# Performance work log

Measured on AMD Instinct MI355X. Metric: run time of the kernel, lower is better.

The kernel has to match this reference:

```python
import jax, jax.numpy as jnp
import numpy as np

# ---- config (matches init_kwargs) ----
B, S, V = 8, 900, 11
H, NH, HD = 512, 8, 64          # hidden, heads, head_dim = H // NH
L = 2                            # num_layers
EXPANSION = 4.0
INNER = 1536                     # find_multiple(round(4.0 * 512 * 2/3), 256)
STEPS = 2                        # mcmc_num_steps
EPS = 1e-5                       # rms_norm_eps
THETA = 10000.0                  # rope_theta
ESCALE = float(np.sqrt(H))       # embed_scale = sqrt(hidden_size)
SCALE = 1.0 / float(np.sqrt(HD))


def rms_norm(x):
    return x * jax.lax.rsqrt(jnp.mean(x * x, axis=-1, keepdims=True) + EPS)


def rope_tables():
    inv_freq = 1.0 / (THETA ** (jnp.arange(0, HD, 2, dtype=jnp.float32) / HD))
    t = jnp.arange(S, dtype=jnp.float32)
    freqs = jnp.outer(t, inv_freq)                # (S, HD/2)
    emb = jnp.concatenate([freqs, freqs], axis=-1)  # (S, HD)
    return jnp.cos(emb), jnp.sin(emb)


def rotate_half(x):
    x1, x2 = jnp.split(x, 2, axis=-1)
    return jnp.concatenate([-x2, x1], axis=-1)


def apply_rope(q, k, cos, sin):
    cos = cos[None, :, None, :]  # (1,S,1,HD) broadcast over batch & heads
    sin = sin[None, :, None, :]
    return q * cos + rotate_half(q) * sin, k * cos + rotate_half(k) * sin


def block(h, qkv_w, o_w, gu_w, d_w, cos, sin):
    b, s, _ = h.shape
    qkv = (h @ qkv_w).reshape(b, s, 3 * NH, HD)
    q, k, v = qkv[:, :, :NH], qkv[:, :, NH:2 * NH], qkv[:, :, 2 * NH:]
    q, k = apply_rope(q, k, cos, sin)
    scores = jnp.einsum('bqhd,bkhd->bhqk', q, k) * SCALE
    attn = jax.nn.softmax(scores, axis=-1)
    out = jnp.einsum('bhqk,bkhd->bqhd', attn, v).reshape(b, s, NH * HD)
    h = rms_norm(h + out @ o_w)                   # post-norm residual
    gu = h @ gu_w
    gate, up = gu[..., :INNER], gu[..., INNER:]
    h = rms_norm(h + (jax.nn.silu(gate) * up) @ d_w)
    return h


def energy(logits, embed_w, energy_w, qkv_w, o_w, gu_w, d_w, input_emb, cos, sin):
    probs = jax.nn.softmax(logits, axis=-1)       # soft token distribution
    h = input_emb + ESCALE * (probs @ embed_w)    # soft embedding
    for i in range(L):
        h = block(h, qkv_w[i], o_w[i], gu_w[i], d_w[i], cos, sin)
    return jnp.sum(h @ energy_w)                  # scalar energy


def setup_inputs() -> dict:
    key = jax.random.key(0)
    ks = jax.random.split(key, 8)
    inputs = jax.random.randint(ks[0], (B, S), 0, V, dtype=jnp.int64)
    puzzle_identifiers = jax.random.randint(ks[1], (B,), 0, 1, dtype=jnp.int64)
    init_std = 1.0 / ESCALE
    embed_w = jax.random.normal(ks[2], (V, H), jnp.float32) * init_std
    energy_w = jax.random.normal(ks[3], (H, 1), jnp.float32) * 0.02
    qkv_w = jax.random.normal(ks[4], (L, H, 3 * NH * HD), jnp.float32) * 0.02
    o_w = jax.random.normal(ks[5], (L, NH * HD, H), jnp.float32) * 0.02
    gu_w = jax.random.normal(ks[6], (L, H, 2 * INNER), jnp.float32) * 0.02
    d_w = jax.random.normal(ks[7], (L, INNER, H), jnp.float32) * 0.02
    alpha = jnp.asarray(100.0, jnp.float32)       # mcmc_step_size
    return {"inputs": inputs, "puzzle_identifiers": puzzle_identifiers,
            "embed_w": embed_w, "energy_w": energy_w, "qkv_w": qkv_w,
            "o_w": o_w, "gu_w": gu_w, "d_w": d_w, "alpha": alpha}


def reference(inputs, puzzle_identifiers, embed_w, energy_w, qkv_w, o_w, gu_w, d_w, alpha):
    cos, sin = rope_tables()
    input_emb = ESCALE * embed_w[inputs]          # (B,S,H)
    a = jnp.maximum(alpha, 1e-4)                  # torch.clamp(alpha, min=1e-4)
    logits = jnp.zeros((inputs.shape[0], S, V), jnp.float32)
    egrad = jax.grad(energy)
    for _ in range(STEPS):                        # MCMC energy-descent loop
        g = egrad(logits, embed_w, energy_w, qkv_w, o_w, gu_w, d_w, input_emb, cos, sin)
        logits = logits - a * g
    return logits
```

## Files before the change

### kernel.cpp

```cpp
#include <hip/hip_runtime.h>
#include <math.h>

#define B_ 8
#define S_ 900
#define V_ 11
#define H_ 512
#define NH_ 8
#define HD_ 64
#define INNER_ 1536
#define STEPS_ 2
#define NTOK (B_*S_)
#define EPS_ 1e-5f
#define THETA_ 10000.0f
#define ESCALE_ 22.627416997969522f
#define SCALE_ 0.125f
#define PT_ 68

typedef __attribute__((ext_vector_type(8))) short bh8;
typedef __attribute__((ext_vector_type(4))) float f32x4;
typedef __attribute__((ext_vector_type(4))) unsigned short us4;

union bfu { bh8 v; unsigned short s[8]; us4 q[2]; };

__device__ inline unsigned short f2bf(float x) {
// ... 74 lines not shown
  if (tid < V_) p[tid] = P[t * V_ + tid];
  if (tid == 0) iw = inp[t];
  __syncthreads();
  for (int h = tid; h < H_; h += blockDim.x) {
    float acc = E[iw * H_ + h];
#pragma unroll
    for (int v = 0; v < V_; ++v) acc += p[v] * E[v * H_ + h];
    float val = ESCALE_ * acc;
    h0[(size_t)t * H_ + h] = val;
    h016[(size_t)t * H_ + h] = f2bf(val);
  }
}

__global__ void k_gfill(const float* __restrict__ ew, float* __restrict__ G) {
  int idx = blockIdx.x * blockDim.x + threadIdx.x;
  if (idx < NTOK * H_) G[idx] = ew[idx & (H_ - 1)];
}

__global__ void k_cast8(const float* __restrict__ X, unsigned short* __restrict__ Y, int n8) {
  int i = blockIdx.x * blockDim.x + threadIdx.x;
  if (i >= n8) return;
  const float4* p = (const float4*)(X + (size_t)i * 8);
  float4 a = p[0], b = p[1];
  bfu o;
  o.s[0] = f2bf(a.x); o.s[1] = f2bf(a.y); o.s[2] = f2bf(a.z); o.s[3] = f2bf(a.w);
  o.s[4] = f2bf(b.x); o.s[5] = f2bf(b.y); o.s[6] = f2bf(b.z); o.s[7] = f2bf(b.w);
  *(bh8*)(Y + (size_t)i * 8) = o.v;
}


__global__ void k_wt(const float* __restrict__ W, unsigned short* __restrict__ WT, int K, int N) {
  __shared__ float t[32][33];
  int k0 = blockIdx.y * 32, n0 = blockIdx.x * 32;
  int tx = threadIdx.x, ty = threadIdx.y;
#pragma unroll
  for (int i = 0; i < 4; ++i)
    t[ty + 8 * i][tx] = W[(size_t)(k0 + ty + 8 * i) * N + n0 + tx];
  __syncthreads();
#pragma unroll
  for (int i = 0; i < 4; ++i)
    WT[(size_t)(n0 + ty + 8 * i) * K + k0 + tx] = f2bf(t[tx][ty + 8 * i]);
}


template <int TM, int SILU_A, int ADD, int CBF, int ROPE, int SILUBWD>
__global__ __launch_bounds__(256) void k_gemm(const unsigned short* __restrict__ A16,
                                              const unsigned short* __restrict__ Bt,
                                              const float* __restrict__ Dm,
                                              float* __restrict__ Cf,
                                              unsigned short* __restrict__ C16,
                                              unsigned short* __restrict__ GU,
                                              const float* __restrict__ Cs,
                                              const float* __restrict__ Sn,
                                              int M, int N, int K, int lda) {
  __shared__ unsigned short As[2][TM][32];
  __shared__ unsigned short Bs[2][128][32];
  constexpr int FR = TM / 32;
  int tid = threadIdx.x;
  int m0 = blockIdx.y * TM, n0 = blockIdx.x * 128;
  int wid = tid >> 6, lane = tid & 63;
  int wr = (wid >> 1) * (FR * 16), wc = (wid & 1) * 64;
  int lr = lane & 15, lg = lane >> 4;
  int srow = lane >> 2, sck = (lane & 3) * 8;
  f32x4 acc[FR][4] = {};
  for (int k0 = 0; k0 < K; k0 += 64) {
    __syncthreads();
#pragma unroll
    for (int sub = 0; sub < 2; ++sub) {
      int kk = k0 + sub * 32;
#pragma unroll
      for (int half = 0; half < TM / 64; ++half) {
        if (SILU_A) {
          int row = (tid >> 2) + 64 * half;
          int ck = (tid & 3) * 8;
          int gr = m0 + row; gr = gr < M ? gr : M - 1;
          const unsigned short* src = &A16[(size_t)gr * lda + kk + ck];
          bfu pa;
#pragma unroll
          for (int j = 0; j < 8; ++j) {
            float g = b2f(src[j]), u = b2f(src[INNER_ + j]);
            pa.s[j] = f2bf((g / (1.f + __expf(-g))) * u);
          }
          *(bh8*)&As[sub][row][ck] = pa.v;
        } else {
          int gr = m0 + 64 * half + wid * 16 + srow; gr = gr < M ? gr : M - 1;
          gld16(&A16[(size_t)gr * lda + kk + sck], &As[sub][64 * half + wid * 16][0]);
        }
      }
#pragma unroll
      for (int i = 0; i < 2; ++i) {
        int bb = wid * 2 + i;
        gld16(&Bt[(size_t)(n0 + bb * 16 + srow) * K + kk + sck], &Bs[sub][bb * 16][0]);
      }
    }
    __syncthreads();
#pragma unroll
    for (int sub = 0; sub < 2; ++sub) {
      bh8 av[FR], bv[4];
#pragma unroll
      for (int fr = 0; fr < FR; ++fr) av[fr] = *(const bh8*)&As[sub][wr + fr * 16 + lr][lg * 8];
#pragma unroll
      for (int fc = 0; fc < 4; ++fc) bv[fc] = *(const bh8*)&Bs[sub][wc + fc * 16 + lr][lg * 8];
#pragma unroll
      for (int fr = 0; fr < FR; ++fr)
#pragma unroll
        for (int fc = 0; fc < 4; ++fc)
          acc[fr][fc] = __builtin_amdgcn_mfma_f32_16x16x32_bf16(av[fr], bv[fc], acc[fr][fc], 0, 0, 0);
    }
  }
  bool rope_on = ROPE && (((n0 + wc) >> 6) < 16);
#pragma unroll
  for (int fr = 0; fr < FR; ++fr) {
    int r0 = m0 + wr + fr * 16 + lg * 4;
#pragma unroll
    for (int i = 0; i < 4; ++i) {
      int gr = r0 + i;
      if (gr >= M) continue;
      float c0 = 1.f, s0 = 0.f, c1 = 1.f, s1 = 0.f;
      if (ROPE) {
        if (rope_on) {
          int s = gr % S_;
          c0 = Cs[s * 32 + lr];      s0 = Sn[s * 32 + lr];
          c1 = Cs[s * 32 + 16 + lr]; s1 = Sn[s * 32 + 16 + lr];
        }
      }
#pragma unroll
      for (int fc = 0; fc < 4; ++fc) {
        int gc = n0 + wc + fc * 16 + lr;
        float out = acc[fr][fc][i];
        if (ROPE) {
          float part = acc[fr][fc ^ 2][i];
          float cc = (fc & 1) ? c1 : c0;
          float ss = (fc & 1) ? s1 : s0;
          out = (fc < 2) ? (out * cc - part * ss) : (out * cc + part * ss);
        }
        if (ADD) out += Dm[(size_t)gr * N + gc];
        if (SILUBWD) {
          size_t gb = (size_t)gr * (size_t)(2 * INNER_) + gc;
          float g = b2f(GU[gb]), u = b2f(GU[gb + INNER_]);
          float sig = 1.f / (1.f + __expf(-g));
          GU[gb] = f2bf(out * u * sig * (1.f + g * (1.f - sig)));
          GU[gb + INNER_] = f2bf(out * g * sig);
        } else if (CBF) {
          C16[(size_t)gr * N + gc] = f2bf(out);
        } else {
          Cf[(size_t)gr * N + gc] = out;
        }
      }
    }
  }
}


__global__ __launch_bounds__(256) void k_attn_fwd3(const unsigned short* __restrict__ QKV,
                                                   unsigned short* __restrict__ AO,
                                                   float* __restrict__ MB,
                                                   float* __restrict__ LB) {
  __shared__ unsigned short Ks[64][PT_];
  __shared__ unsigned short VT[64][PT_];
  __shared__ unsigned short Ps[4][16][PT_];
  int tid = threadIdx.x;
  int h = blockIdx.y, b = blockIdx.z;
  int w = tid >> 6, lane = tid & 63;
  int lr = lane & 15, lg = lane >> 4;
  int q0 = blockIdx.x * 64 + w * 16;
  int sr = tid >> 2, sc0 = (tid & 3) * 16;
  int vd0 = (tid & 15) * 4, vk0 = (tid >> 4) * 4;

  bh8 qf[2];
  {
    int qr = q0 + lr; if (qr >= S_) qr = S_ - 1;
    const unsigned short* qp = &QKV[((size_t)(b * S_ + qr) * 24 + h) * 64 + lg * 8];
    qf[0] = *(const bh8*)qp;
    qf[1] = *(const bh8*)(qp + 32);
  }
  f32x4 accO[4] = {};
  float m[4], lsum[4];
#pragma unroll
  for (int i = 0; i < 4; ++i) { m[i] = -1e30f; lsum[i] = 0.f; }

  bfu kA, kB;
  us4 vR[4];
  {
    int src = sr;
    size_t ts = (size_t)b * S_ + (src < S_ ? src : S_ - 1);
    const unsigned short* gp = &QKV[(ts * 24 + 8 + h) * 64 + sc0];
    kA.v = *(const bh8*)gp;
    kB.v = *(const bh8*)(gp + 8);
#pragma unroll
    for (int j = 0; j < 4; ++j) {
      int s2 = vk0 + j;
      size_t t2 = (size_t)b * S_ + (s2 < S_ ? s2 : S_ - 1);
      vR[j] = *(const us4*)&QKV[(t2 * 24 + 16 + h) * 64 + vd0];
    }
  }

  for (int kt = 0; kt < S_; kt += 64) {
    __syncthreads();
    sts16(&Ks[sr][sc0], kA);
    sts16(&Ks[sr][sc0 + 8], kB);
#pragma unroll
    for (int dd = 0; dd < 4; ++dd) {
      us4 pk = {vR[0][dd], vR[1][dd], vR[2][dd], vR[3][dd]};
      *(us4*)&VT[vd0 + dd][vk0] = pk;
    }
    __syncthreads();
    if (kt + 64 < S_) {
      int src = kt + 64 + sr;
      size_t ts = (size_t)b * S_ + (src < S_ ? src : S_ - 1);
      const unsigned short* gp = &QKV[(ts * 24 + 8 + h) * 64 + sc0];
      kA.v = *(const bh8*)gp;
      kB.v = *(const bh8*)(gp + 8);
#pragma unroll
      for (int j = 0; j < 4; ++j) {
        int s2 = kt + 64 + vk0 + j;
        size_t t2 = (size_t)b * S_ + (s2 < S_ ? s2 : S_ - 1);
        vR[j] = *(const us4*)&QKV[(t2 * 24 + 16 + h) * 64 + vd0];
      }
    }
    f32x4 accS[4] = {};
#pragma unroll
    for (int ks = 0; ks < 2; ++ks)
#pragma unroll
      for (int fk = 0; fk < 4; ++fk)
        accS[fk] = __builtin_amdgcn_mfma_f32_16x16x32_bf16(qf[ks], lds16(&Ks[fk * 16 + lr][ks * 32 + lg * 8]), accS[fk], 0, 0, 0);
    float sc[4][4], pmax[4];
#pragma unroll
    for (int i = 0; i < 4; ++i) pmax[i] = -1e30f;
#pragma unroll
    for (int fk = 0; fk < 4; ++fk)
#pragma unroll
      for (int i = 0; i < 4; ++i) {
        float s = accS[fk][i] * SCALE_;
        if (kt + fk * 16 + lr >= S_) s = -1e30f;
        sc[fk][i] = s;
        pmax[i] = fmaxf(pmax[i], s);
      }
#pragma unroll
    for (int i = 0; i < 4; ++i) {
      float v = pmax[i];
      v = fmaxf(v, __shfl_xor(v, 1, 64));
      v = fmaxf(v, __shfl_xor(v, 2, 64));
      v = fmaxf(v, __shfl_xor(v, 4, 64));
      v = fmaxf(v, __shfl_xor(v, 8, 64));
      pmax[i] = v;
    }
    float psum[4];
#pragma unroll
    for (int i = 0; i < 4; ++i) {
      float mn = fmaxf(m[i], pmax[i]);
      float eo = __expf(m[i] - mn);
      m[i] = mn;
      lsum[i] *= eo;
#pragma unroll
      for (int fd = 0; fd < 4; ++fd) accO[fd][i] *= eo;
      psum[i] = 0.f;
    }
#pragma unroll
    for (int fk = 0; fk < 4; ++fk)
#pragma unroll
      for (int i = 0; i < 4; ++i) {
        float p = __expf(sc[fk][i] - m[i]);
        sc[fk][i] = p;
        psum[i] += p;
      }
#pragma unroll
    for (int i = 0; i < 4; ++i) {
      float v = psum[i];
      v += __shfl_xor(v, 1, 64);
      v += __shfl_xor(v, 2, 64);
      v += __shfl_xor(v, 4, 64);
      v += __shfl_xor(v, 8, 64);
      lsum[i] += v;
    }
#pragma unroll
    for (int fk = 0; fk < 4; ++fk)
#pragma unroll
      for (int i = 0; i < 4; ++i)
        Ps[w][lg * 4 + i][fk * 16 + lr] = f2bf(sc[fk][i]);
#pragma unroll
    for (int ks = 0; ks < 2; ++ks) {
      bh8 ap = lds16(&Ps[w][lr][ks * 32 + lg * 8]);
#pragma unroll
      for (int fd = 0; fd < 4; ++fd)
        accO[fd] = __builtin_amdgcn_mfma_f32_16x16x32_bf16(ap, lds16(&VT[fd * 16 + lr][ks * 32 + lg * 8]), accO[fd], 0, 0, 0);
    }
  }
#pragma unroll
  for (int i = 0; i < 4; ++i) {
    int q = q0 + lg * 4 + i;
    if (q < S_) {
      float linv = 1.f / lsum[i];
      size_t obase = (size_t)(b * S_ + q) * H_ + h * 64;
#pragma unroll
      for (int fd = 0; fd < 4; ++fd) AO[obase + fd * 16 + lr] = f2bf(accO[fd][i] * linv);
      if (lr == 0) {
        MB[((size_t)b * NH_ + h) * S_ + q] = m[i];
        LB[((size_t)b * NH_ + h) * S_ + q] = linv;
      }
    }
  }
}

__global__ __launch_bounds__(256) void k_delta(const unsigned short* __restrict__ O,
                                               const unsigned short* __restrict__ dO,
                                               float* __restrict__ DB) {
  int tid = threadIdx.x;
  int h = blockIdx.y, b = blockIdx.z;
  int r = blockIdx.x * 64 + (tid >> 2), part = tid & 3;
  if (r >= S_) return;
  size_t base = (size_t)(b * S_ + r) * H_ + h * 64 + part * 16;
  bfu o0, o1, d0, d1;
  o0.v = *(const bh8*)&O[base];  o1.v = *(const bh8*)&O[base + 8];
  d0.v = *(const bh8*)&dO[base]; d1.v = *(const bh8*)&dO[base + 8];
  float s = 0.f;
#pragma unroll
  for (int j = 0; j < 8; ++j)
    s += b2f(o0.s[j]) * b2f(d0.s[j]) + b2f(o1.s[j]) * b2f(d1.s[j]);
  s = quad_sum(s);
  if (part == 0) DB[((size_t)b * NH_ + h) * S_ + r] = s;
}

__global__ __launch_bounds__(256) void k_attn_bwd_dq3(const unsigned short* __restrict__ QKV,
                                                      const unsigned short* __restrict__ dO,
                                                      const float* __restrict__ MB,
                                                      const float* __restrict__ LB,
                                                      const float* __restrict__ DB,
                                                      const float* __restrict__ Cs,
                                                      const float* __restrict__ Sn,
                                                      unsigned short* __restrict__ dQKV) {
  __shared__ unsigned short Ks[64][PT_];
  __shared__ unsigned short Vs[64][PT_];
  __shared__ unsigned short KT[64][PT_];
  __shared__ unsigned short Ps[4][16][PT_];
  int tid = threadIdx.x;
  int h = blockIdx.y, b = blockIdx.z;
  int w = tid >> 6, lane = tid & 63;
  int lr = lane & 15, lg = lane >> 4;
  int q0 = blockIdx.x * 64 + w * 16;
  size_t sbase = ((size_t)b * NH_ + h) * S_;
  int sr = tid >> 2, sc0 = (tid & 3) * 16;
  int vd0 = (tid & 15) * 4, vk0 = (tid >> 4) * 4;

  bh8 qf[2], dof[2];
  {
    int qr = q0 + lr; if (qr >= S_) qr = S_ - 1;
    const unsigned short* qp = &QKV[((size_t)(b * S_ + qr) * 24 + h) * 64 + lg * 8];
    const unsigned short* dp = &dO[(size_t)(b * S_ + qr) * H_ + h * 64 + lg * 8];
    qf[0] = *(const bh8*)qp;  qf[1] = *(const bh8*)(qp + 32);
    dof[0] = *(const bh8*)dp; dof[1] = *(const bh8*)(dp + 32);
  }
  float mrow[4], lrow[4], drow[4];
#pragma unroll
  for (int i = 0; i < 4; ++i) {
    int q = q0 + lg * 4 + i; if (q >= S_) q = S_ - 1;
    mrow[i] = MB[sbase + q];
    lrow[i] = LB[sbase + q];
    drow[i] = DB[sbase + q];
  }
  f32x4 accQ[4] = {};

  bfu pA{}, pB{}, pC{}, pD{};
  us4 rv[4];
  {
    int src = sr;
    bool vld = src < S_;
    size_t ts = (size_t)b * S_ + (vld ? src : S_ - 1);
    const unsigned short* kp = &QKV[(ts * 24 + 8 + h) * 64 + sc0];
    if (vld) {
      pA.v = *(const bh8*)kp;
      pB.v = *(const bh8*)(kp + 8);
      pC.v = *(const bh8*)(kp + 512);
      pD.v = *(const bh8*)(kp + 520);
    }
#pragma unroll
    for (int j = 0; j < 4; ++j) {
      int s2 = vk0 + j;
      bool v2 = s2 < S_;
      size_t t2 = (size_t)b * S_ + (v2 ? s2 : S_ - 1);
      us4 t = *(const us4*)&QKV[(t2 * 24 + 8 + h) * 64 + vd0];
      if (!v2) t = us4{0, 0, 0, 0};
      rv[j] = t;
    }
  }

  for (int kt = 0; kt < S_; kt += 64) {
    __syncthreads();
    sts16(&Ks[sr][sc0], pA); sts16(&Ks[sr][sc0 + 8], pB);
    sts16(&Vs[sr][sc0], pC); sts16(&Vs[sr][sc0 + 8], pD);
#pragma unroll
    for (int dd = 0; dd < 4; ++dd) {
      us4 pk = {rv[0][dd], rv[1][dd], rv[2][dd], rv[3][dd]};
      *(us4*)&KT[vd0 + dd][vk0] = pk;
    }
    __syncthreads();
    if (kt + 64 < S_) {
      int src = kt + 64 + sr;
      bool vld = src < S_;
      size_t ts = (size_t)b * S_ + (vld ? src : S_ - 1);
      const unsigned short* kp = &QKV[(ts * 24 + 8 + h) * 64 + sc0];
      pA = bfu{}; pB = bfu{}; pC = bfu{}; pD = bfu{};
      if (vld) {
        pA.v = *(const bh8*)kp;
        pB.v = *(const bh8*)(kp + 8);
        pC.v = *(const bh8*)(kp + 512);
        pD.v = *(const bh8*)(kp + 520);
      }
#pragma unroll
      for (int j = 0; j < 4; ++j) {
        int s2 = kt + 64 + vk0 + j;
        bool v2 = s2 < S_;
        size_t t2 = (size_t)b * S_ + (v2 ? s2 : S_ - 1);
        us4 t = *(const us4*)&QKV[(t2 * 24 + 8 + h) * 64 + vd0];
        if (!v2) t = us4{0, 0, 0, 0};
        rv[j] = t;
      }
    }
    f32x4 aS[4] = {}, aD[4] = {};
#pragma unroll
    for (int ks = 0; ks < 2; ++ks)
#pragma unroll
      for (int fk = 0; fk < 4; ++fk) {
        aS[fk] = __builtin_amdgcn_mfma_f32_16x16x32_bf16(qf[ks], lds16(&Ks[fk * 16 + lr][ks * 32 + lg * 8]), aS[fk], 0, 0, 0);
        aD[fk] = __builtin_amdgcn_mfma_f32_16x16x32_bf16(dof[ks], lds16(&Vs[fk * 16 + lr][ks * 32 + lg * 8]), aD[fk], 0, 0, 0);
      }
#pragma unroll
    for (int fk = 0; fk < 4; ++fk)
#pragma unroll
      for (int i = 0; i < 4; ++i) {
        float p = __expf(aS[fk][i] * SCALE_ - mrow[i]) * lrow[i];
        float ds = p * (aD[fk][i] - drow[i]);
        Ps[w][lg * 4 + i][fk * 16 + lr] = f2bf(ds);
      }
#pragma unroll
    for (int ks = 0; ks < 2; ++ks) {
      bh8 ap = lds16(&Ps[w][lr][ks * 32 + lg * 8]);
#pragma unroll
      for (int fd = 0; fd < 4; ++fd)
        accQ[fd] = __builtin_amdgcn_mfma_f32_16x16x32_bf16(ap, lds16(&KT[fd * 16 + lr][ks * 32 + lg * 8]), accQ[fd], 0, 0, 0);
    }
  }
#pragma unroll
  for (int i = 0; i < 4; ++i) {
    int q = q0 + lg * 4 + i;
    if (q < S_) {
      size_t obase = ((size_t)(b * S_ + q) * 24 + h) * 64;
      float c0 = Cs[q * 32 + lr], s0 = Sn[q * 32 + lr];
      float c1 = Cs[q * 32 + 16 + lr], s1 = Sn[q * 32 + 16 + lr];
#pragma unroll
      for (int fd = 0; fd < 4; ++fd) {
        float x = SCALE_ * accQ[fd][i];
        float p = SCALE_ * accQ[fd ^ 2][i];
        float cc = (fd & 1) ? c1 : c0;
        float ss = (fd & 1) ? s1 : s0;
        float out = (fd < 2) ? (x * cc + p * ss) : (x * cc - p * ss);
        dQKV[obase + fd * 16 + lr] = f2bf(out);
      }
    }
  }
}

__global__ __launch_bounds__(256) void k_attn_bwd_kv3(const unsigned short* __restrict__ QKV,
                                                      const unsigned short* __restrict__ dO,
                                                      const float* __restrict__ MB,
                                                      const float* __restrict__ LB,
                                                      const float* __restrict__ DB,
                                                      const float* __restrict__ Cs,
                                                      const float* __restrict__ Sn,
                                                      unsigned short* __restrict__ dQKV) {
  __shared__ unsigned short Qs[64][PT_];
  __shared__ unsigned short dOs[64][PT_];
  __shared__ unsigned short QT[64][PT_];
  __shared__ unsigned short dOT[64][PT_];
  __shared__ unsigned short Ps[4][16][PT_];
  __shared__ float sM[64], sL[64], sD[64];
  int tid = threadIdx.x;
  int h = blockIdx.y, b = blockIdx.z;
  int w = tid >> 6, lane = tid & 63;
  int lr = lane & 15, lg = lane >> 4;
  int k0w = blockIdx.x * 64 + w * 16;
  size_t sbase = ((size_t)b * NH_ + h) * S_;
  int sr = tid >> 2, sc0 = (tid & 3) * 16;
  int vd0 = (tid & 15) * 4, vk0 = (tid >> 4) * 4;

  bh8 kf[2], vf[2];
  {
    int kr = k0w + lr; if (kr >= S_) kr = S_ - 1;
    const unsigned short* kp = &QKV[((size_t)(b * S_ + kr) * 24 + 8 + h) * 64 + lg * 8];
    kf[0] = *(const bh8*)kp;        kf[1] = *(const bh8*)(kp + 32);
    vf[0] = *(const bh8*)(kp + 512); vf[1] = *(const bh8*)(kp + 544);
  }
  f32x4 accK[4] = {}, accV[4] = {};

  bfu pA, pB, pC{}, pD{};
  us4 rq[4], rd[4];
  float stM = 0.f, stL = 0.f, stD = 0.f;
  {
    int src = sr;
    bool vld = src < S_;
    size_t ts = (size_t)b * S_ + (vld ? src : S_ - 1);
    const unsigned short* qp = &QKV[(ts * 24 + h) * 64 + sc0];
    const unsigned short* dp = &dO[ts * H_ + h * 64 + sc0];
    pA.v = *(const bh8*)qp;
    pB.v = *(const bh8*)(qp + 8);
    if (vld) {
      pC.v = *(const bh8*)dp;
      pD.v = *(const bh8*)(dp + 8);
    }
#pragma unroll
    for (int j = 0; j < 4; ++j) {
      int s2 = vk0 + j;
      bool v2 = s2 < S_;
      size_t t2 = (size_t)b * S_ + (v2 ? s2 : S_ - 1);
      rq[j] = *(const us4*)&QKV[(t2 * 24 + h) * 64 + vd0];
      us4 td = *(const us4*)&dO[t2 * H_ + h * 64 + vd0];
      if (!v2) td = us4{0, 0, 0, 0};
      rd[j] = td;
    }
    if (tid < 64) {
      bool v2 = tid < S_;
      int sc = v2 ? tid : S_ - 1;
      stM = MB[sbase + sc];
      stL = LB[sbase + sc];
      stD = v2 ? DB[sbase + sc] : 0.f;
    }
  }

  for (int qt = 0; qt < S_; qt += 64) {
    __syncthreads();
    sts16(&Qs[sr][sc0], pA);  sts16(&Qs[sr][sc0 + 8], pB);
    sts16(&dOs[sr][sc0], pC); sts16(&dOs[sr][sc0 + 8], pD);
#pragma unroll
    for (int dd = 0; dd < 4; ++dd) {
      us4 pq = {rq[0][dd], rq[1][dd], rq[2][dd], rq[3][dd]};
      us4 pd = {rd[0][dd], rd[1][dd], rd[2][dd], rd[3][dd]};
      *(us4*)&QT[vd0 + dd][vk0] = pq;
      *(us4*)&dOT[vd0 + dd][vk0] = pd;
    }
    if (tid < 64) {
      sM[tid] = stM;
      sL[tid] = stL;
      sD[tid] = stD;
    }
    __syncthreads();
    if (qt + 64 < S_) {
      int src = qt + 64 + sr;
      bool vld = src < S_;
      size_t ts = (size_t)b * S_ + (vld ? src : S_ - 1);
      const unsigned short* qp = &QKV[(ts * 24 + h) * 64 + sc0];
      const unsigned short* dp = &dO[ts * H_ + h * 64 + sc0];
      pA.v = *(const bh8*)qp;
      pB.v = *(const bh8*)(qp + 8);
      pC = bfu{}; pD = bfu{};
      if (vld) {
        pC.v = *(const bh8*)dp;
        pD.v = *(const bh8*)(dp + 8);
      }
#pragma unroll
      for (int j = 0; j < 4; ++j) {
        int s2 = qt + 64 + vk0 + j;
        bool v2 = s2 < S_;
        size_t t2 = (size_t)b * S_ + (v2 ? s2 : S_ - 1);
        rq[j] = *(const us4*)&QKV[(t2 * 24 + h) * 64 + vd0];
        us4 td = *(const us4*)&dO[t2 * H_ + h * 64 + vd0];
        if (!v2) td = us4{0, 0, 0, 0};
        rd[j] = td;
      }
      if (tid < 64) {
        int s2 = qt + 64 + tid;
        bool v2 = s2 < S_;
        int sc = v2 ? s2 : S_ - 1;
        stM = MB[sbase + sc];
        stL = LB[sbase + sc];
        stD = v2 ? DB[sbase + sc] : 0.f;
      }
    }
    f32x4 aS[4] = {}, aD[4] = {};
#pragma unroll
    for (int ks = 0; ks < 2; ++ks)
#pragma unroll
      for (int fq = 0; fq < 4; ++fq) {
        aS[fq] = __builtin_amdgcn_mfma_f32_16x16x32_bf16(kf[ks], lds16(&Qs[fq * 16 + lr][ks * 32 + lg * 8]), aS[fq], 0, 0, 0);
        aD[fq] = __builtin_amdgcn_mfma_f32_16x16x32_bf16(vf[ks], lds16(&dOs[fq * 16 + lr][ks * 32 + lg * 8]), aD[fq], 0, 0, 0);
      }
    float pv[4][4];
#pragma unroll
    for (int fq = 0; fq < 4; ++fq) {
      float mq = sM[fq * 16 + lr], lq = sL[fq * 16 + lr];
#pragma unroll
      for (int i = 0; i < 4; ++i) {
        float p = __expf(aS[fq][i] * SCALE_ - mq) * lq;
        pv[fq][i] = p;
        Ps[w][lg * 4 + i][fq * 16 + lr] = f2bf(p);
      }
    }
#pragma unroll
    for (int qs = 0; qs < 2; ++qs) {
      bh8 ap = lds16(&Ps[w][lr][qs * 32 + lg * 8]);
#pragma unroll
      for (int fd = 0; fd < 4; ++fd)
        accV[fd] = __builtin_amdgcn_mfma_f32_16x16x32_bf16(ap, lds16(&dOT[fd * 16 + lr][qs * 32 + lg * 8]), accV[fd], 0, 0, 0);
    }
#pragma unroll
    for (int fq = 0; fq < 4; ++fq) {
      float dq = sD[fq * 16 + lr];
#pragma unroll
      for (int i = 0; i < 4; ++i)
        Ps[w][lg * 4 + i][fq * 16 + lr] = f2bf(pv[fq][i] * (aD[fq][i] - dq));
    }
#pragma unroll
    for (int qs = 0; qs < 2; ++qs) {
      bh8 ap = lds16(&Ps[w][lr][qs * 32 + lg * 8]);
#pragma unroll
      for (int fd = 0; fd < 4; ++fd)
        accK[fd] = __builtin_amdgcn_mfma_f32_16x16x32_bf16(ap, lds16(&QT[fd * 16 + lr][qs * 32 + lg * 8]), accK[fd], 0, 0, 0);
    }
  }
#pragma unroll
  for (int i = 0; i < 4; ++i) {
    int k = k0w + lg * 4 + i;
    if (k < S_) {
      size_t obase = ((size_t)(b * S_ + k) * 24 + 8 + h) * 64;
      float c0 = Cs[k * 32 + lr], s0 = Sn[k * 32 + lr];
      float c1 = Cs[k * 32 + 16 + lr], s1 = Sn[k * 32 + 16 + lr];
#pragma unroll
      for (int fd = 0; fd < 4; ++fd) {
        float x = SCALE_ * accK[fd][i];
        float p = SCALE_ * accK[fd ^ 2][i];
        float cc = (fd & 1) ? c1 : c0;
        float ss = (fd & 1) ? s1 : s0;
        float out = (fd < 2) ? (x * cc + p * ss) : (x * cc - p * ss);
        dQKV[obase + fd * 16 + lr] = f2bf(out);
        dQKV[obase + 512 + fd * 16 + lr] = f2bf(accV[fd][i]);
      }
    }
  }
}


__global__ __launch_bounds__(256) void k_rms_fwd(const float* __restrict__ X, float* __restrict__ Y,
                                                 unsigned short* __restrict__ Y16) {
  int t = blockIdx.x, tid = threadIdx.x;
  float x0 = X[(size_t)t * H_ + tid], x1 = X[(size_t)t * H_ + tid + 256];
  __shared__ float red[256];
  red[tid] = x0 * x0 + x1 * x1;
  __syncthreads();
  for (int s = 128; s > 0; s >>= 1) {
    if (tid < s) red[tid] += red[tid + s];
    __syncthreads();
  }
  float r = rsqrtf(red[0] / H_ + EPS_);
  float y0 = x0 * r, y1 = x1 * r;
  Y[(size_t)t * H_ + tid] = y0;
  Y[(size_t)t * H_ + tid + 256] = y1;
  Y16[(size_t)t * H_ + tid] = f2bf(y0);
  Y16[(size_t)t * H_ + tid + 256] = f2bf(y1);
}

__global__ __launch_bounds__(256) void k_rms_bwd(const float* __restrict__ X,
                                                 const float* __restrict__ GY,
                                                 float* __restrict__ GX,
                                                 unsigned short* __restrict__ GX16) {
  int t = blockIdx.x, tid = threadIdx.x;
  float x0 = X[(size_t)t * H_ + tid], x1 = X[(size_t)t * H_ + tid + 256];
  float g0 = GY[(size_t)t * H_ + tid], g1 = GY[(size_t)t * H_ + tid + 256];
  __shared__ float r1[256], r2[256];
  r1[tid] = x0 * x0 + x1 * x1;
  r2[tid] = x0 * g0 + x1 * g1;
  __syncthreads();
  for (int s = 128; s > 0; s >>= 1) {
    if (tid < s) { r1[tid] += r1[tid + s]; r2[tid] += r2[tid + s]; }
    __syncthreads();
  }
  float r = rsqrtf(r1[0] / H_ + EPS_);
  float coef = r * r * r * r2[0] / (float)H_;
  float o0 = r * g0 - coef * x0, o1 = r * g1 - coef * x1;
  GX[(size_t)t * H_ + tid] = o0;
  GX[(size_t)t * H_ + tid + 256] = o1;
  GX16[(size_t)t * H_ + tid] = f2bf(o0);
  GX16[(size_t)t * H_ + tid + 256] = f2bf(o1);
}


__global__ __launch_bounds__(64) void k_logits_update(const float* __restrict__ G,
                                                      const float* __restrict__ E,
                                                      const float* __restrict__ P,
                                                      const float* __restrict__ alpha,
                                                      float* __restrict__ logits) {
  int t = blockIdx.x, lane = threadIdx.x;
  float dp[V_];
#pragma unroll
  for (int v = 0; v < V_; ++v) dp[v] = 0.f;
  for (int hh = lane; hh < H_; hh += 64) {
    float gh = G[(size_t)t * H_ + hh];
#pragma unroll
    for (int v = 0; v < V_; ++v) dp[v] += gh * E[v * H_ + hh];
  }
#pragma unroll
  for (int v = 0; v < V_; ++v) dp[v] = wave_sum64(dp[v]) * ESCALE_;
  float dot = 0.f;
  float pv[V_];
#pragma unroll
  for (int v = 0; v < V_; ++v) {
    pv[v] = P[t * V_ + v];
    dot += pv[v] * dp[v];
  }
  float a = fmaxf(alpha[0], 1e-4f);
  if (lane < V_) logits[t * V_ + lane] -= a * pv[lane] * (dp[lane] - dot);
}


struct Ctx {
  unsigned short *Q16, *Q016, *dQ16, *GU16, *DO16, *AO16, *AO016, *X116, *UDX16, *U016;
  float *X1, *X2, *X20, *G, *UDX, *P, *MB, *LB, *DB, *MB0, *LB0, *CS, *SN;
  const unsigned short *WTqkv[2], *WTo[2], *WTgu[2], *WTd[2];
  const unsigned short *WSqkv[2], *WSo[2], *WSgu[2], *WSd[2];
  hipStream_t st;
};

static void block_forward(Ctx& c, int l, const float* hin, const unsigned short* hin16,
                          float* hout, unsigned short* qb, unsigned short* ao,
                          float* mb, float* lb, float* x2buf, unsigned short* u16buf) {
  k_gemm<128, 0, 0, 1, 1, 0><<<dim3(3 * H_ / 128, (NTOK + 127) / 128), 256, 0, c.st>>>(
      hin16, c.WTqkv[l], nullptr, nullptr, qb, nullptr, c.CS, c.SN, NTOK, 3 * H_, H_, H_);
  k_attn_fwd3<<<dim3((S_ + 63) / 64, NH_, B_), 256, 0, c.st>>>(qb, ao, mb, lb);
  k_gemm<64, 0, 1, 0, 0, 0><<<dim3(H_ / 128, (NTOK + 63) / 64), 256, 0, c.st>>>(
      ao, c.WTo[l], hin, c.X1, nullptr, nullptr, nullptr, nullptr, NTOK, H_, H_, H_);
  k_rms_fwd<<<NTOK, 256, 0, c.st>>>(c.X1, c.UDX, u16buf);
  k_gemm<128, 0, 0, 1, 0, 0><<<dim3(2 * INNER_ / 128, (NTOK + 127) / 128), 256, 0, c.st>>>(
      u16buf, c.WTgu[l], nullptr, nullptr, c.GU16, nullptr, nullptr, nullptr, NTOK, 2 * INNER_, H_, H_);
  k_gemm<64, 1, 1, 0, 0, 0><<<dim3(H_ / 128, (NTOK + 63) / 64), 256, 0, c.st>>>(
      c.GU16, c.WTd[l], c.UDX, x2buf, nullptr, nullptr, nullptr, nullptr, NTOK, H_, INNER_, 2 * INNER_);
  if (hout) k_rms_fwd<<<NTOK, 256, 0, c.st>>>(x2buf, hout, c.UDX16);
}

static void block_backward(Ctx& c, int l, const float* hin, const unsigned short* hin16,
                           unsigned short* qb, unsigned short* ao, float* mb, float* lb,
                           bool full) {
  const float* x2src;
  if (full) {
    block_forward(c, l, hin, hin16, nullptr, qb, ao, mb, lb, c.X2, c.UDX16);
    x2src = c.X2;
  } else {
    k_gemm<64, 0, 1, 0, 0, 0><<<dim3(H_ / 128, (NTOK + 63) / 64), 256, 0, c.st>>>(
        ao, c.WTo[l], hin, c.X1, nullptr, nullptr, nullptr, nullptr, NTOK, H_, H_, H_);
    k_gemm<128, 0, 0, 1, 0, 0><<<dim3(2 * INNER_ / 128, (NTOK + 127) / 128), 256, 0, c.st>>>(
        c.U016, c.WTgu[l], nullptr, nullptr, c.GU16, nullptr, nullptr, nullptr, NTOK, 2 * INNER_, H_, H_);
    x2src = c.X20;
  }
  k_rms_bwd<<<NTOK, 256, 0, c.st>>>(x2src, c.G, c.UDX, c.UDX16);
  k_gemm<128, 0, 0, 0, 0, 1><<<dim3(INNER_ / 128, (NTOK + 127) / 128), 256, 0, c.st>>>(
      c.UDX16, c.WSd[l], nullptr, nullptr, nullptr, c.GU16, nullptr, nullptr, NTOK, INNER_, H_, H_);
  k_gemm<64, 0, 1, 0, 0, 0><<<dim3(H_ / 128, (NTOK + 63) / 64), 256, 0, c.st>>>(
      c.GU16, c.WSgu[l], c.UDX, c.G, nullptr, nullptr, nullptr, nullptr, NTOK, H_, 2 * INNER_, 2 * INNER_);
  k_rms_bwd<<<NTOK, 256, 0, c.st>>>(c.X1, c.G, c.UDX, c.UDX16);
  k_gemm<64, 0, 0, 1, 0, 0><<<dim3(H_ / 128, (NTOK + 63) / 64), 256, 0, c.st>>>(
      c.UDX16, c.WSo[l], nullptr, nullptr, c.DO16, nullptr, nullptr, nullptr, NTOK, H_, H_, H_);
  dim3 agrid((S_ + 63) / 64, NH_, B_);
  k_delta<<<agrid, 256, 0, c.st>>>(ao, c.DO16, c.DB);
  k_attn_bwd_dq3<<<agrid, 256, 0, c.st>>>(qb, c.DO16, mb, lb, c.DB, c.CS, c.SN, c.dQ16);
  k_attn_bwd_kv3<<<agrid, 256, 0, c.st>>>(qb, c.DO16, mb, lb, c.DB, c.CS, c.SN, c.dQ16);
  k_gemm<64, 0, 1, 0, 0, 0><<<dim3(H_ / 128, (NTOK + 63) / 64), 256, 0, c.st>>>(
      c.dQ16, c.WSqkv[l], c.UDX, c.G, nullptr, nullptr, nullptr, nullptr, NTOK, H_, 3 * H_, 3 * H_);
}

extern "C" void kernel_launch(void* const* d_in, const int* in_sizes, int n_in,
                              void* d_out, int out_size, void* d_ws, size_t ws_size,
                              hipStream_t stream) {
  const int* inputs = (const int*)d_in[0];
  const float* E = (const float*)d_in[2];
  const float* ew = (const float*)d_in[3];
  const float* qkvw = (const float*)d_in[4];
  const float* ow = (const float*)d_in[5];
  const float* guw = (const float*)d_in[6];
  const float* dw = (const float*)d_in[7];
  const float* alpha = (const float*)d_in[8];
  float* logits = (float*)d_out;

  const size_t WT_FLOATS = 3407872;
  const size_t NEED =
      3 * ((size_t)NTOK * 3 * H_ / 2) +
      ((size_t)NTOK * INNER_) +
      5 * ((size_t)NTOK * H_) +
      6 * ((size_t)NTOK * H_ / 2) +
      ((size_t)NTOK * V_) +
      5 * ((size_t)B_ * NH_ * S_) +
      2 * ((size_t)S_ * 32) +
      2 * WT_FLOATS;
  if (ws_size < NEED * sizeof(float)) {
    k_zero<<<(NTOK * V_ + 255) / 256, 256, 0, stream>>>(logits, NTOK * V_);
    return;
  }

  float* f = (float*)d_ws;
  Ctx c;
  c.st = stream;
  c.Q16 = (unsigned short*)f;  f += (size_t)NTOK * 3 * H_ / 2;
  c.Q016 = (unsigned short*)f; f += (size_t)NTOK * 3 * H_ / 2;
  c.dQ16 = (unsigned short*)f; f += (size_t)NTOK * 3 * H_ / 2;
  c.GU16 = (unsigned short*)f; f += (size_t)NTOK * INNER_;
  c.X1 = f;   f += (size_t)NTOK * H_;
  c.X2 = f;   f += (size_t)NTOK * H_;
  c.X20 = f;  f += (size_t)NTOK * H_;
  c.G = f;    f += (size_t)NTOK * H_;
  c.UDX = f;  f += (size_t)NTOK * H_;
  c.AO16 = (unsigned short*)f;  f += (size_t)NTOK * H_ / 2;
  c.AO016 = (unsigned short*)f; f += (size_t)NTOK * H_ / 2;
  c.DO16 = (unsigned short*)f;  f += (size_t)NTOK * H_ / 2;
  c.X116 = (unsigned short*)f;  f += (size_t)NTOK * H_ / 2;
  c.UDX16 = (unsigned short*)f; f += (size_t)NTOK * H_ / 2;
  c.U016 = (unsigned short*)f;  f += (size_t)NTOK * H_ / 2;
  c.P = f;    f += (size_t)NTOK * V_;
  c.MB = f;   f += (size_t)B_ * NH_ * S_;
  c.LB = f;   f += (size_t)B_ * NH_ * S_;
  c.DB = f;   f += (size_t)B_ * NH_ * S_;
  c.MB0 = f;  f += (size_t)B_ * NH_ * S_;
  c.LB0 = f;  f += (size_t)B_ * NH_ * S_;
  c.CS = f;   f += (size_t)S_ * 32;
  c.SN = f;   f += (size_t)S_ * 32;
  unsigned short* wt = (unsigned short*)f;

  const size_t LQKV = (size_t)H_ * 3 * H_;
  const size_t LO = (size_t)H_ * H_;
  const size_t LGU = (size_t)H_ * 2 * INNER_;
  const size_t LD = (size_t)INNER_ * H_;

  for (int l = 0; l < 2; ++l) {
    c.WTqkv[l] = wt;
    k_wt<<<dim3(3 * H_ / 32, H_ / 32), dim3(32, 8), 0, stream>>>(qkvw + l * LQKV, wt, H_, 3 * H_);
    wt += LQKV;
    c.WTo[l] = wt;
    k_wt<<<dim3(H_ / 32, H_ / 32), dim3(32, 8), 0, stream>>>(ow + l * LO, wt, H_, H_);
    wt += LO;
    c.WTgu[l] = wt;
    k_wt<<<dim3(2 * INNER_ / 32, H_ / 32), dim3(32, 8), 0, stream>>>(guw + l * LGU, wt, H_, 2 * INNER_);
    wt += LGU;
    c.WTd[l] = wt;
    k_wt<<<dim3(H_ / 32, INNER_ / 32), dim3(32, 8), 0, stream>>>(dw + l * LD, wt, INNER_, H_);
    wt += LD;
  }
  {
    unsigned short* ws = wt;
    k_cast8<<<(int)((2 * LQKV / 8 + 255) / 256), 256, 0, stream>>>(qkvw, ws, (int)(2 * LQKV / 8));
    c.WSqkv[0] = ws; c.WSqkv[1] = ws + LQKV; ws += 2 * LQKV;
    k_cast8<<<(int)((2 * LO / 8 + 255) / 256), 256, 0, stream>>>(ow, ws, (int)(2 * LO / 8));
    c.WSo[0] = ws; c.WSo[1] = ws + LO; ws += 2 * LO;
    k_cast8<<<(int)((2 * LGU / 8 + 255) / 256), 256, 0, stream>>>(guw, ws, (int)(2 * LGU / 8));
    c.WSgu[0] = ws; c.WSgu[1] = ws + LGU; ws += 2 * LGU;
    k_cast8<<<(int)((2 * LD / 8 + 255) / 256), 256, 0, stream>>>(dw, ws, (int)(2 * LD / 8));
    c.WSd[0] = ws; c.WSd[1] = ws + LD;
  }

  k_zero<<<(NTOK * V_ + 255) / 256, 256, 0, stream>>>(logits, NTOK * V_);
  k_rope_tables<<<(S_ * 32 + 255) / 256, 256, 0, stream>>>(c.CS, c.SN);

  for (int step = 0; step < STEPS_; ++step) {
    k_softmax_logits<<<(NTOK + 255) / 256, 256, 0, stream>>>(logits, c.P);
    k_h0<<<NTOK, 256, 0, stream>>>(c.P, E, inputs, c.X1, c.X116);
    block_forward(c, 0, c.X1, c.X116, c.UDX, c.Q016, c.AO016, c.MB0, c.LB0, c.X20, c.U016);
    k_gfill<<<(NTOK * H_ + 255) / 256, 256, 0, stream>>>(ew, c.G);
    block_backward(c, 1, c.UDX, c.UDX16, c.Q16, c.AO16, c.MB, c.LB, true);
    k_h0<<<NTOK, 256, 0, stream>>>(c.P, E, inputs, c.X1, c.X116);
    block_backward(c, 0, c.X1, c.X116, c.Q016, c.AO016, c.MB0, c.LB0, false);
    k_logits_update<<<NTOK, 64, 0, stream>>>(c.G, E, c.P, alpha, logits);
  }
}
```

Measured before the change: 2.356 ms.

## Double attention query tile to 128 rows with 512-thread blocks and split K/V staging roles

The forward, dQ and dKV attention kernels now run 8 waves per block over 128 query (or key) rows instead of 4 waves over 64. Each K/V tile staged in shared memory is therefore reused by twice as many waves. The staging work is split so the first 256 threads load the row-major tile and the other 256 build the transposed tile, which halves the per-thread load work. In exchange there are fewer blocks (8 per head instead of 15), a larger tail on the last tile, and more register and shared-memory pressure at 512 threads per block.

```diff
diff --git a/kernel.cpp b/kernel.cpp
--- a/kernel.cpp
+++ b/kernel.cpp
@@ -250,20 +250,22 @@
 }
 
 
-__global__ __launch_bounds__(256) void k_attn_fwd3(const unsigned short* __restrict__ QKV,
+__global__ __launch_bounds__(512) void k_attn_fwd3(const unsigned short* __restrict__ QKV,
                                                    unsigned short* __restrict__ AO,
                                                    float* __restrict__ MB,
                                                    float* __restrict__ LB) {
   __shared__ unsigned short Ks[64][PT_];
   __shared__ unsigned short VT[64][PT_];
-  __shared__ unsigned short Ps[4][16][PT_];
+  __shared__ unsigned short Ps[8][16][PT_];
   int tid = threadIdx.x;
   int h = blockIdx.y, b = blockIdx.z;
   int w = tid >> 6, lane = tid & 63;
   int lr = lane & 15, lg = lane >> 4;
-  int q0 = blockIdx.x * 64 + w * 16;
-  int sr = tid >> 2, sc0 = (tid & 3) * 16;
-  int vd0 = (tid & 15) * 4, vk0 = (tid >> 4) * 4;
+  int q0 = blockIdx.x * 128 + w * 16;
+  bool kRole = tid < 256;
+  int t2 = kRole ? tid : tid - 256;
+  int sr = t2 >> 2, sc0 = (t2 & 3) * 16;
+  int vd0 = (t2 & 15) * 4, vk0 = (t2 >> 4) * 4;
 
   bh8 qf[2];
   {
@@ -279,41 +281,48 @@
 
   bfu kA, kB;
   us4 vR[4];
-  {
+  if (kRole) {
     int src = sr;
     size_t ts = (size_t)b * S_ + (src < S_ ? src : S_ - 1);
     const unsigned short* gp = &QKV[(ts * 24 + 8 + h) * 64 + sc0];
     kA.v = *(const bh8*)gp;
     kB.v = *(const bh8*)(gp + 8);
+  } else {
 #pragma unroll
     for (int j = 0; j < 4; ++j) {
       int s2 = vk0 + j;
-      size_t t2 = (size_t)b * S_ + (s2 < S_ ? s2 : S_ - 1);
-      vR[j] = *(const us4*)&QKV[(t2 * 24 + 16 + h) * 64 + vd0];
+      size_t t3 = (size_t)b * S_ + (s2 < S_ ? s2 : S_ - 1);
+      vR[j] = *(const us4*)&QKV[(t3 * 24 + 16 + h) * 64 + vd0];
     }
   }
 
   for (int kt = 0; kt < S_; kt += 64) {
     __syncthreads();
-    sts16(&Ks[sr][sc0], kA);
-    sts16(&Ks[sr][sc0 + 8], kB);
-#pragma unroll
-    for (int dd = 0; dd < 4; ++dd) {
-      us4 pk = {vR[0][dd], vR[1][dd], vR[2][dd], vR[3][dd]};
-      *(us4*)&VT[vd0 + dd][vk0] = pk;
+    if (kRole) {
+      sts16(&Ks[sr][sc0], kA);
+      sts16(&Ks[sr][sc0 + 8], kB);
+    } else {
+#pragma unroll
+      for (int dd = 0; dd < 4; ++dd) {
+        us4 pk = {vR[0][dd], vR[1][dd], vR[2][dd], vR[3][dd]};
+        *(us4*)&VT[vd0 + dd][vk0] = pk;
+      }
     }
     __syncthreads();
     if (kt + 64 < S_) {
-      int src = kt + 64 + sr;
-      size_t ts = (size_t)b * S_ + (src < S_ ? src : S_ - 1);
-      const unsigned short* gp = &QKV[(ts * 24 + 8 + h) * 64 + sc0];
-      kA.v = *(const bh8*)gp;
-      kB.v = *(const bh8*)(gp + 8);
-#pragma unroll
-      for (int j = 0; j < 4; ++j) {
-        int s2 = kt + 64 + vk0 + j;
-        size_t t2 = (size_t)b * S_ + (s2 < S_ ? s2 : S_ - 1);
-        vR[j] = *(const us4*)&QKV[(t2 * 24 + 16 + h) * 64 + vd0];
+      if (kRole) {
+        int src = kt + 64 + sr;
+        size_t ts = (size_t)b * S_ + (src < S_ ? src : S_ - 1);
+        const unsigned short* gp = &QKV[(ts * 24 + 8 + h) * 64 + sc0];
+        kA.v = *(const bh8*)gp;
+        kB.v = *(const bh8*)(gp + 8);
+      } else {
+#pragma unroll
+        for (int j = 0; j < 4; ++j) {
+          int s2 = kt + 64 + vk0 + j;
+          size_t t3 = (size_t)b * S_ + (s2 < S_ ? s2 : S_ - 1);
+          vR[j] = *(const us4*)&QKV[(t3 * 24 + 16 + h) * 64 + vd0];
+        }
       }
     }
     f32x4 accS[4] = {};
@@ -419,7 +428,7 @@
   if (part == 0) DB[((size_t)b * NH_ + h) * S_ + r] = s;
 }
 
-__global__ __launch_bounds__(256) void k_attn_bwd_dq3(const unsigned short* __restrict__ QKV,
+__global__ __launch_bounds__(512) void k_attn_bwd_dq3(const unsigned short* __restrict__ QKV,
                                                       const unsigned short* __restrict__ dO,
                                                       const float* __restrict__ MB,
                                                       const float* __restrict__ LB,
@@ -430,15 +439,17 @@
   __shared__ unsigned short Ks[64][PT_];
   __shared__ unsigned short Vs[64][PT_];
   __shared__ unsigned short KT[64][PT_];
-  __shared__ unsigned short Ps[4][16][PT_];
+  __shared__ unsigned short Ps[8][16][PT_];
   int tid = threadIdx.x;
   int h = blockIdx.y, b = blockIdx.z;
   int w = tid >> 6, lane = tid & 63;
   int lr = lane & 15, lg = lane >> 4;
-  int q0 = blockIdx.x * 64 + w * 16;
+  int q0 = blockIdx.x * 128 + w * 16;
   size_t sbase = ((size_t)b * NH_ + h) * S_;
-  int sr = tid >> 2, sc0 = (tid & 3) * 16;
-  int vd0 = (tid & 15) * 4, vk0 = (tid >> 4) * 4;
+  bool kRole = tid < 256;
+  int t2 = kRole ? tid : tid - 256;
+  int sr = t2 >> 2, sc0 = (t2 & 3) * 16;
+  int vd0 = (t2 & 15) * 4, vk0 = (t2 >> 4) * 4;
 
   bh8 qf[2], dof[2];
   {
@@ -460,7 +471,7 @@
 
   bfu pA{}, pB{}, pC{}, pD{};
   us4 rv[4];
-  {
+  if (kRole) {
     int src = sr;
     bool vld = src < S_;
     size_t ts = (size_t)b * S_ + (vld ? src : S_ - 1);
@@ -471,12 +482,13 @@
       pC.v = *(const bh8*)(kp + 512);
       pD.v = *(const bh8*)(kp + 520);
     }
+  } else {
 #pragma unroll
     for (int j = 0; j < 4; ++j) {
       int s2 = vk0 + j;
       bool v2 = s2 < S_;
-      size_t t2 = (size_t)b * S_ + (v2 ? s2 : S_ - 1);
-      us4 t = *(const us4*)&QKV[(t2 * 24 + 8 + h) * 64 + vd0];
+      size_t t3 = (size_t)b * S_ + (v2 ? s2 : S_ - 1);
+      us4 t = *(const us4*)&QKV[(t3 * 24 + 8 + h) * 64 + vd0];
       if (!v2) t = us4{0, 0, 0, 0};
       rv[j] = t;
     }
@@ -484,34 +496,40 @@
 
   for (int kt = 0; kt < S_; kt += 64) {
     __syncthreads();
-    sts16(&Ks[sr][sc0], pA); sts16(&Ks[sr][sc0 + 8], pB);
-    sts16(&Vs[sr][sc0], pC); sts16(&Vs[sr][sc0 + 8], pD);
-#pragma unroll
-    for (int dd = 0; dd < 4; ++dd) {
-      us4 pk = {rv[0][dd], rv[1][dd], rv[2][dd], rv[3][dd]};
-      *(us4*)&KT[vd0 + dd][vk0] = pk;
+    if (kRole) {
+      sts16(&Ks[sr][sc0], pA); sts16(&Ks[sr][sc0 + 8], pB);
+      sts16(&Vs[sr][sc0], pC); sts16(&Vs[sr][sc0 + 8], pD);
+    } else {
+#pragma unroll
+      for (int dd = 0; dd < 4; ++dd) {
+        us4 pk = {rv[0][dd], rv[1][dd], rv[2][dd], rv[3][dd]};
+        *(us4*)&KT[vd0 + dd][vk0] = pk;
+      }
     }
     __syncthreads();
     if (kt + 64 < S_) {
-      int src = kt + 64 + sr;
-      bool vld = src < S_;
-      size_t ts = (size_t)b * S_ + (vld ? src : S_ - 1);
-      const unsigned short* kp = &QKV[(ts * 24 + 8 + h) * 64 + sc0];
-      pA = bfu{}; pB = bfu{}; pC = bfu{}; pD = bfu{};
-      if (vld) {
-        pA.v = *(const bh8*)kp;
-        pB.v = *(const bh8*)(kp + 8);
-        pC.v = *(const bh8*)(kp + 512);
-        pD.v = *(const bh8*)(kp + 520);
-      }
-#pragma unroll
-      for (int j = 0; j < 4; ++j) {
-        int s2 = kt + 64 + vk0 + j;
-        bool v2 = s2 < S_;
-        size_t t2 = (size_t)b * S_ + (v2 ? s2 : S_ - 1);
-        us4 t = *(const us4*)&QKV[(t2 * 24 + 8 + h) * 64 + vd0];
-        if (!v2) t = us4{0, 0, 0, 0};
-        rv[j] = t;
+      if (kRole) {
+        int src = kt + 64 + sr;
+        bool vld = src < S_;
+        size_t ts = (size_t)b * S_ + (vld ? src : S_ - 1);
+        const unsigned short* kp = &QKV[(ts * 24 + 8 + h) * 64 + sc0];
+        pA = bfu{}; pB = bfu{}; pC = bfu{}; pD = bfu{};
+        if (vld) {
+          pA.v = *(const bh8*)kp;
+          pB.v = *(const bh8*)(kp + 8);
+          pC.v = *(const bh8*)(kp + 512);
+          pD.v = *(const bh8*)(kp + 520);
+        }
+      } else {
+#pragma unroll
+        for (int j = 0; j < 4; ++j) {
+          int s2 = kt + 64 + vk0 + j;
+          bool v2 = s2 < S_;
+          size_t t3 = (size_t)b * S_ + (v2 ? s2 : S_ - 1);
+          us4 t = *(const us4*)&QKV[(t3 * 24 + 8 + h) * 64 + vd0];
+          if (!v2) t = us4{0, 0, 0, 0};
+          rv[j] = t;
+        }
       }
     }
     f32x4 aS[4] = {}, aD[4] = {};
@@ -558,7 +576,7 @@
   }
 }
 
-__global__ __launch_bounds__(256) void k_attn_bwd_kv3(const unsigned short* __restrict__ QKV,
+__global__ __launch_bounds__(512) void k_attn_bwd_kv3(const unsigned short* __restrict__ QKV,
                                                       const unsigned short* __restrict__ dO,
                                                       const float* __restrict__ MB,
                                                       const float* __restrict__ LB,
@@ -570,16 +588,18 @@
   __shared__ unsigned short dOs[64][PT_];
   __shared__ unsigned short QT[64][PT_];
   __shared__ unsigned short dOT[64][PT_];
-  __shared__ unsigned short Ps[4][16][PT_];
+  __shared__ unsigned short Ps[8][16][PT_];
   __shared__ float sM[64], sL[64], sD[64];
   int tid = threadIdx.x;
   int h = blockIdx.y, b = blockIdx.z;
   int w = tid >> 6, lane = tid & 63;
   int lr = lane & 15, lg = lane >> 4;
-  int k0w = blockIdx.x * 64 + w * 16;
+  int k0w = blockIdx.x * 128 + w * 16;
   size_t sbase = ((size_t)b * NH_ + h) * S_;
-  int sr = tid >> 2, sc0 = (tid & 3) * 16;
-  int vd0 = (tid & 15) * 4, vk0 = (tid >> 4) * 4;
+  bool kRole = tid < 256;
+  int t2 = kRole ? tid : tid - 256;
+  int sr = t2 >> 2, sc0 = (t2 & 3) * 16;
+  int vd0 = (t2 & 15) * 4, vk0 = (t2 >> 4) * 4;
 
   bh8 kf[2], vf[2];
   {
@@ -590,10 +610,10 @@
   }
   f32x4 accK[4] = {}, accV[4] = {};
 
-  bfu pA, pB, pC{}, pD{};
+  bfu pA{}, pB{}, pC{}, pD{};
   us4 rq[4], rd[4];
   float stM = 0.f, stL = 0.f, stD = 0.f;
-  {
+  if (kRole) {
     int src = sr;
     bool vld = src < S_;
     size_t ts = (size_t)b * S_ + (vld ? src : S_ - 1);
@@ -605,16 +625,6 @@
       pC.v = *(const bh8*)dp;
       pD.v = *(const bh8*)(dp + 8);
     }
-#pragma unroll
-    for (int j = 0; j < 4; ++j) {
-      int s2 = vk0 + j;
-      bool v2 = s2 < S_;
-      size_t t2 = (size_t)b * S_ + (v2 ? s2 : S_ - 1);
-      rq[j] = *(const us4*)&QKV[(t2 * 24 + h) * 64 + vd0];
-      us4 td = *(const us4*)&dO[t2 * H_ + h * 64 + vd0];
-      if (!v2) td = us4{0, 0, 0, 0};
-      rd[j] = td;
-    }
     if (tid < 64) {
       bool v2 = tid < S_;
       int sc = v2 ? tid : S_ - 1;
@@ -622,55 +632,72 @@
       stL = LB[sbase + sc];
       stD = v2 ? DB[sbase + sc] : 0.f;
     }
+  } else {
+#pragma unroll
+    for (int j = 0; j < 4; ++j) {
+      int s2 = vk0 + j;
+      bool v2 = s2 < S_;
+      size_t t3 = (size_t)b * S_ + (v2 ? s2 : S_ - 1);
+      rq[j] = *(const us4*)&QKV[(t3 * 24 + h) * 64 + vd0];
+      us4 td = *(const us4*)&dO[t3 * H_ + h * 64 + vd0];
+      if (!v2) td = us4{0, 0, 0, 0};
+      rd[j] = td;
+    }
   }
 
   for (int qt = 0; qt < S_; qt += 64) {
     __syncthreads();
-    sts16(&Qs[sr][sc0], pA);  sts16(&Qs[sr][sc0 + 8], pB);
-    sts16(&dOs[sr][sc0], pC); sts16(&dOs[sr][sc0 + 8], pD);
-#pragma unroll
-    for (int dd = 0; dd < 4; ++dd) {
-      us4 pq = {rq[0][dd], rq[1][dd], rq[2][dd], rq[3][dd]};
-      us4 pd = {rd[0][dd], rd[1][dd], rd[2][dd], rd[3][dd]};
-      *(us4*)&QT[vd0 + dd][vk0] = pq;
-      *(us4*)&dOT[vd0 + dd][vk0] = pd;
-    }
-    if (tid < 64) {
-      sM[tid] = stM;
-      sL[tid] = stL;
-      sD[tid] = stD;
+    if (kRole) {
+      sts16(&Qs[sr][sc0], pA);  sts16(&Qs[sr][sc0 + 8], pB);
+      sts16(&dOs[sr][sc0], pC); sts16(&dOs[sr][sc0 + 8], pD);
+      if (tid < 64) {
+        sM[tid] = stM;
+        sL[tid] = stL;
+        sD[tid] = stD;
+      }
+    } else {
+#pragma unroll
+      for (int dd = 0; dd < 4; ++dd) {
+        us4 pq = {rq[0][dd], rq[1][dd], rq[2][dd], rq[3][dd]};
+        us4 pd = {rd[0][dd], rd[1][dd], rd[2][dd], rd[3][dd]};
+        *(us4*)&QT[vd0 + dd][vk0] = pq;
+        *(us4*)&dOT[vd0 + dd][vk0] = pd;
+      }
     }
     __syncthreads();
     if (qt + 64 < S_) {
-      int src = qt + 64 + sr;
-      bool vld = src < S_;
-      size_t ts = (size_t)b * S_ + (vld ? src : S_ - 1);
-      const unsigned short* qp = &QKV[(ts * 24 + h) * 64 + sc0];
-      const unsigned short* dp = &dO[ts * H_ + h * 64 + sc0];
-      pA.v = *(const bh8*)qp;
-      pB.v = *(const bh8*)(qp + 8);
-      pC = bfu{}; pD = bfu{};
-      if (vld) {
-        pC.v = *(const bh8*)dp;
-        pD.v = *(const bh8*)(dp + 8);
-      }
-#pragma unroll
-      for (int j = 0; j < 4; ++j) {
-        int s2 = qt + 64 + vk0 + j;
-        bool v2 = s2 < S_;
-        size_t t2 = (size_t)b * S_ + (v2 ? s2 : S_ - 1);
-        rq[j] = *(const us4*)&QKV[(t2 * 24 + h) * 64 + vd0];
-        us4 td = *(const us4*)&dO[t2 * H_ + h * 64 + vd0];
-        if (!v2) td = us4{0, 0, 0, 0};
-        rd[j] = td;
-      }
-      if (tid < 64) {
-        int s2 = qt + 64 + tid;
-        bool v2 = s2 < S_;
-        int sc = v2 ? s2 : S_ - 1;
-        stM = MB[sbase + sc];
-        stL = LB[sbase + sc];
-        stD = v2 ? DB[sbase + sc] : 0.f;
+      if (kRole) {
+        int src = qt + 64 + sr;
+        bool vld = src < S_;
+        size_t ts = (size_t)b * S_ + (vld ? src : S_ - 1);
+        const unsigned short* qp = &QKV[(ts * 24 + h) * 64 + sc0];
+        const unsigned short* dp = &dO[ts * H_ + h * 64 + sc0];
+        pA.v = *(const bh8*)qp;
+        pB.v = *(const bh8*)(qp + 8);
+        pC = bfu{}; pD = bfu{};
+        if (vld) {
+          pC.v = *(const bh8*)dp;
+          pD.v = *(const bh8*)(dp + 8);
+        }
+        if (tid < 64) {
+          int s2 = qt + 64 + tid;
+          bool v2 = s2 < S_;
+          int sc = v2 ? s2 : S_ - 1;
+          stM = MB[sbase + sc];
+          stL = LB[sbase + sc];
+          stD = v2 ? DB[sbase + sc] : 0.f;
+        }
+      } else {
+#pragma unroll
+        for (int j = 0; j < 4; ++j) {
+          int s2 = qt + 64 + vk0 + j;
+          bool v2 = s2 < S_;
+          size_t t3 = (size_t)b * S_ + (v2 ? s2 : S_ - 1);
+          rq[j] = *(const us4*)&QKV[(t3 * 24 + h) * 64 + vd0];
+          us4 td = *(const us4*)&dO[t3 * H_ + h * 64 + vd0];
+          if (!v2) td = us4{0, 0, 0, 0};
+          rd[j] = td;
+        }
       }
     }
     f32x4 aS[4] = {}, aD[4] = {};
@@ -821,7 +848,7 @@
                           float* mb, float* lb, float* x2buf, unsigned short* u16buf) {
   k_gemm<128, 0, 0, 1, 1, 0><<<dim3(3 * H_ / 128, (NTOK + 127) / 128), 256, 0, c.st>>>(
       hin16, c.WTqkv[l], nullptr, nullptr, qb, nullptr, c.CS, c.SN, NTOK, 3 * H_, H_, H_);
-  k_attn_fwd3<<<dim3((S_ + 63) / 64, NH_, B_), 256, 0, c.st>>>(qb, ao, mb, lb);
+  k_attn_fwd3<<<dim3((S_ + 127) / 128, NH_, B_), 512, 0, c.st>>>(qb, ao, mb, lb);
   k_gemm<64, 0, 1, 0, 0, 0><<<dim3(H_ / 128, (NTOK + 63) / 64), 256, 0, c.st>>>(
       ao, c.WTo[l], hin, c.X1, nullptr, nullptr, nullptr, nullptr, NTOK, H_, H_, H_);
   k_rms_fwd<<<NTOK, 256, 0, c.st>>>(c.X1, c.UDX, u16buf);
@@ -854,10 +881,11 @@
   k_rms_bwd<<<NTOK, 256, 0, c.st>>>(c.X1, c.G, c.UDX, c.UDX16);
   k_gemm<64, 0, 0, 1, 0, 0><<<dim3(H_ / 128, (NTOK + 63) / 64), 256, 0, c.st>>>(
       c.UDX16, c.WSo[l], nullptr, nullptr, c.DO16, nullptr, nullptr, nullptr, NTOK, H_, H_, H_);
-  dim3 agrid((S_ + 63) / 64, NH_, B_);
-  k_delta<<<agrid, 256, 0, c.st>>>(ao, c.DO16, c.DB);
-  k_attn_bwd_dq3<<<agrid, 256, 0, c.st>>>(qb, c.DO16, mb, lb, c.DB, c.CS, c.SN, c.dQ16);
-  k_attn_bwd_kv3<<<agrid, 256, 0, c.st>>>(qb, c.DO16, mb, lb, c.DB, c.CS, c.SN, c.dQ16);
+  dim3 agrid64((S_ + 63) / 64, NH_, B_);
+  dim3 agrid128((S_ + 127) / 128, NH_, B_);
+  k_delta<<<agrid64, 256, 0, c.st>>>(ao, c.DO16, c.DB);
+  k_attn_bwd_dq3<<<agrid128, 512, 0, c.st>>>(qb, c.DO16, mb, lb, c.DB, c.CS, c.SN, c.dQ16);
+  k_attn_bwd_kv3<<<agrid128, 512, 0, c.st>>>(qb, c.DO16, mb, lb, c.DB, c.CS, c.SN, c.dQ16);
   k_gemm<64, 0, 1, 0, 0, 0><<<dim3(H_ / 128, (NTOK + 63) / 64), 256, 0, c.st>>>(
       c.dQ16, c.WSqkv[l], c.UDX, c.G, nullptr, nullptr, nullptr, nullptr, NTOK, H_, 3 * H_, 3 * H_);
 }
```

New measurement: 2.291 ms. -2.8%, faster.
